# Performance work log

Hardware: AMD Instinct MI355X
Metric: run time of the kernel (lower is better)

The kernel has to match this reference:

```python
import jax, jax.numpy as jnp
import numpy as np
from jax.scipy.special import gammaln, digamma

V, H, K, B = 50000, 100, 50, 2048
BN_EPS = 1e-5
SAMPLE_KEY = jax.random.key(42)  # fixed key standing in for Dirichlet rsample noise


def setup_inputs() -> dict:
    key = jax.random.key(0)
    ks = jax.random.split(key, 6)
    def lin(k, fan_in, fan_out):
        bound = 1.0 / np.sqrt(fan_in)
        return jax.random.uniform(k, (fan_in, fan_out), jnp.float32, -bound, bound)
    return {
        'input_bows': jax.random.uniform(ks[0], (B, V), jnp.float32),  # BoW features
        'W1': lin(ks[1], V, H), 'b1': jnp.zeros((H,), jnp.float32),
        'W2': lin(ks[2], H, H), 'b2': jnp.zeros((H,), jnp.float32),
        'Wt': lin(ks[3], H, K), 'bt': jnp.zeros((K,), jnp.float32),
        'bn_gamma': jnp.ones((K,), jnp.float32), 'bn_beta': jnp.zeros((K,), jnp.float32),
        'Wd': lin(ks[4], K, V), 'bd': jnp.zeros((V,), jnp.float32),
    }


def reference(input_bows, W1, b1, W2, b2, Wt, bt, bn_gamma, bn_beta, Wd, bd):
    # --- MLP encoder: Linear -> Softplus, Linear -> Softplus ---
    h = jax.nn.softplus(input_bows @ W1 + b1)        # [B, H]
    h = jax.nn.softplus(h @ W2 + b2)                  # [B, H]
    # --- h2t: Linear -> BatchNorm1d (training-mode batch stats) -> exp ---
    t = h @ Wt + bt                                   # [B, K]
    mu = jnp.mean(t, axis=0)
    var = jnp.mean((t - mu) ** 2, axis=0)             # biased variance (torch BN)
    t_hat = (t - mu) * jax.lax.rsqrt(var + BN_EPS) * bn_gamma + bn_beta
    alpha = jnp.exp(t_hat)                            # Dirichlet concentration [B, K]
    # --- Dirichlet rsample: normalized Gamma (reparameterized) ---
    g = jax.random.gamma(SAMPLE_KEY, alpha)           # [B, K]
    sample = g / jnp.sum(g, axis=-1, keepdims=True)
    # --- decode: Linear -> log_softmax ---
    logits = jax.nn.log_softmax(sample @ Wd + bd, axis=-1)  # [B, V]
    rec_loss = -jnp.sum(logits * input_bows, axis=1)        # [B]
    # --- KL( Dirichlet(alpha) || Dirichlet(1) ) ---
    a0 = jnp.sum(alpha, axis=-1)                            # [B]
    kld = (gammaln(a0) - jnp.sum(gammaln(alpha), axis=-1) - gammaln(jnp.float32(K))
           + jnp.sum((alpha - 1.0) * (digamma(alpha) - digamma(a0)[:, None]), axis=-1))
    return sample, logits, kld, rec_loss
```

## Files before the change

### kernel.cpp

```cpp
#include <hip/hip_runtime.h>
#include <cstdint>
#include <cstddef>

#define DEV __device__ __forceinline__

struct TFKey { uint32_t a, b; };

DEV uint32_t rotl32(uint32_t x, uint32_t r){ return (x << r) | (x >> (32u - r)); }

DEV TFKey tf2x32(TFKey k, uint32_t x0, uint32_t x1){
  uint32_t ks0 = k.a, ks1 = k.b, ks2 = k.a ^ k.b ^ 0x1BD11BDAu;
  x0 += ks0; x1 += ks1;
  x0 += x1; x1 = rotl32(x1,13); x1 ^= x0;
  x0 += x1; x1 = rotl32(x1,15); x1 ^= x0;
  x0 += x1; x1 = rotl32(x1,26); x1 ^= x0;
  x0 += x1; x1 = rotl32(x1, 6); x1 ^= x0;
  x0 += ks1; x1 += ks2 + 1u;
  x0 += x1; x1 = rotl32(x1,17); x1 ^= x0;
  x0 += x1; x1 = rotl32(x1,29); x1 ^= x0;
  x0 += x1; x1 = rotl32(x1,16); x1 ^= x0;
  x0 += x1; x1 = rotl32(x1,24); x1 ^= x0;
  x0 += ks2; x1 += ks0 + 2u;
  x0 += x1; x1 = rotl32(x1,13); x1 ^= x0;
  x0 += x1; x1 = rotl32(x1,15); x1 ^= x0;
  x0 += x1; x1 = rotl32(x1,26); x1 ^= x0;
  x0 += x1; x1 = rotl32(x1, 6); x1 ^= x0;
  x0 += ks0; x1 += ks1 + 3u;
  x0 += x1; x1 = rotl32(x1,17); x1 ^= x0;
  x0 += x1; x1 = rotl32(x1,29); x1 ^= x0;
  x0 += x1; x1 = rotl32(x1,16); x1 ^= x0;
  x0 += x1; x1 = rotl32(x1,24); x1 ^= x0;
  x0 += ks1; x1 += ks2 + 4u;
  x0 += x1; x1 = rotl32(x1,13); x1 ^= x0;
  x0 += x1; x1 = rotl32(x1,15); x1 ^= x0;
  x0 += x1; x1 = rotl32(x1,26); x1 ^= x0;
  x0 += x1; x1 = rotl32(x1, 6); x1 ^= x0;
  x0 += ks2; x1 += ks0 + 5u;
  return TFKey{x0, x1};
}

DEV TFKey tf_child(TFKey k, uint32_t i){ return tf2x32(k, 0u, i); }
DEV uint32_t rb32(TFKey k){ TFKey o = tf2x32(k, 0u, 0u); return o.a ^ o.b; }

DEV float u01(TFKey k){
  uint32_t bits = rb32(k);
  return __uint_as_float((bits >> 9) | 0x3F800000u) - 1.0f;
}

DEV float cr_logf(float x){ return (float)log((double)x); }
DEV float cr_expf(float x){ return (float)exp((double)x); }
DEV float cr_powf(float x, float y){ return (float)pow((double)x, (double)y); }

DEV float xla_erfinv(float x){
  #pragma clang fp contract(off)
  float w = -(float)log1p((double)(-(x*x)));
  float p;
  if (w < 5.0f){
    w = w - 2.5f;
    p = 2.81022636e-08f;
    p = 3.43273939e-07f + p*w;
    p = -3.5233877e-06f + p*w;
    p = -4.39150654e-06f + p*w;
    p = 0.00021858087f  + p*w;
    p = -0.00125372503f + p*w;
    p = -0.00417768164f + p*w;
    p = 0.246640727f    + p*w;
    p = 1.50140941f     + p*w;
  } else {
    w = sqrtf(w) - 3.0f;
    p = -0.000200214257f;
    p = 0.000100950558f + p*w;
    p = 0.00134934322f  + p*w;
    p = -0.00367342844f + p*w;
    p = 0.00573950773f  + p*w;
    p = -0.0076224613f  + p*w;
    p = 0.00943887047f  + p*w;
    p = 1.00167406f     + p*w;
    p = 2.83297682f     + p*w;
  }
  return p*x;
}

DEV float normal_f(TFKey k){
  #pragma clang fp contract(off)
  uint32_t bits = rb32(k);
  float f = __uint_as_float((bits >> 9) | 0x3F800000u) - 1.0f;
  const float lo = -0x1.fffffep-1f;
  float u = f*2.0f + lo;
  u = fmaxf(lo, u);
  return 0x1.6a09e6p+0f * xla_erfinv(u);
}

DEV float gamma_one(TFKey ek, float alpha){
  #pragma clang fp contract(off)
  TFKey key = tf_child(ek, 0u);
  TFKey sub = tf_child(ek, 1u);
  bool bm = (alpha >= 1.0f);
  float a_orig = alpha;
  float ab = bm ? alpha : (alpha + 1.0f);
  const float c13 = 0x1.555556p-2f;
  float d = ab - c13;
  float c = c13 / sqrtf(d);
  float X = 0.0f, Vv = 1.0f, U = 2.0f;
  for (int it = 0; it < 1000; ++it){
    float sq = 1.0f - 0.0331f*(X*X);
    bool cont = false;
    if (U >= sq){
      float lV  = cr_logf(Vv);
      float rhs = 0.5f*X + ((d - d*Vv) + d*lV);
      cont = (cr_logf(U) >= rhs);
    }
    if (!cont) break;
    TFKey nk = tf_child(key, 0u);
    TFKey xk = tf_child(key, 1u);
    TFKey Uk = tf_child(key, 2u);
    key = nk;
    float x = 0.0f, v = -1.0f;
    for (int j = 0; j < 1000 && v <= 0.0f; ++j){
      TFKey nx = tf_child(xk, 0u);
      TFKey sk = tf_child(xk, 1u);
      xk = nx;
      x = normal_f(sk);
      v = 1.0f + x*c;
    }
    X = x*x;
    Vv = (v*v)*v;
    U = u01(Uk);
  }
  float boost = 1.0f;
  if (!bm) boost = cr_powf(u01(sub), 1.0f / a_orig);
  return (d*Vv)*boost;
}

DEV double digamma_d(double x){
  double r = 0.0;
  while (x < 6.0){ r -= 1.0/x; x += 1.0; }
  double ix = 1.0/x, ix2 = ix*ix;
  double ser = ix2*(1.0/12 - ix2*(1.0/120 - ix2*(1.0/252 - ix2*(1.0/240 - ix2*(1.0/132)))));
  return r + log(x) - 0.5*ix - ser;
}

DEV float softplus_cr(float x){
  double xd = (double)x;
  if (x > 0.0f) return (float)(xd + log1p(exp(-xd)));
  return (float)log1p(exp(xd));
}

__global__ __launch_bounds__(256) void k1_gemm(const float* __restrict__ bows,
                                               const float* __restrict__ W1,
                                               float* __restrict__ pre_part){
  __shared__ float4 At4[64*20];
  int rowb = blockIdx.x * 64;
  int kb   = blockIdx.y * 400;
  int tid  = threadIdx.x;
  int c    = tid & 31;
  int r8   = tid >> 5;
  float acc[8][4] = {};
  int cols[4];
  #pragma unroll
  for (int j = 0; j < 4; ++j){ int col = c + 32*j; cols[j] = col < 100 ? col : 96; }
  for (int t = 0; t < 5; ++t){
    int k0 = kb + t*80;
    #pragma unroll
    for (int j = 0; j < 5; ++j){
      int idx = tid + 256*j;
      int r = idx / 20, kf = idx - 20*r;
      At4[idx] = *(const float4*)(bows + (size_t)(rowb + r)*50000 + k0 + kf*4);
    }
    __syncthreads();
    const float* wbase = W1 + (size_t)k0 * 100;
    #pragma unroll 4
    for (int k4 = 0; k4 < 80; k4 += 4){
      float4 a[8];
      #pragma unroll
      for (int i = 0; i < 8; ++i) a[i] = At4[(r8 + 8*i)*20 + (k4 >> 2)];
      #pragma unroll
      for (int kk = 0; kk < 4; ++kk){
        const float* wr = wbase + (size_t)(k4 + kk)*100;
        float w[4];
        #pragma unroll
        for (int j = 0; j < 4; ++j) w[j] = wr[cols[j]];
        #pragma unroll
        for (int i = 0; i < 8; ++i){
          float av = (kk == 0) ? a[i].x : (kk == 1) ? a[i].y : (kk == 2) ? a[i].z : a[i].w;
          #pragma unroll
          for (int j = 0; j < 4; ++j) acc[i][j] = fmaf(av, w[j], acc[i][j]);
        }
      }
    }
    __syncthreads();
  }
  float* pp = pre_part + (size_t)blockIdx.y * 204800;
  #pragma unroll
  for (int i = 0; i < 8; ++i)
    #pragma unroll
    for (int j = 0; j < 4; ++j){
      int col = c + 32*j;
      if (col < 100) pp[(size_t)(rowb + r8 + 8*i)*100 + col] = acc[i][j];
    }
}

__global__ void k2a(const float* __restrict__ pre_part, const float* __restrict__ b1,
                    float* __restrict__ h1){
  int idx = blockIdx.x*256 + threadIdx.x;
  float s = 0.0f;
  #pragma unroll 5
  for (int sp = 0; sp < 125; ++sp) s += pre_part[(size_t)sp*204800 + idx];
  s += b1[idx % 100];
  h1[idx] = softplus_cr(s);
}

__global__ void k2b(const float* __restrict__ h1, const float* __restrict__ W2,
                    const float* __restrict__ b2, float* __restrict__ h2){
  int idx = blockIdx.x*256 + threadIdx.x;
  int row = idx / 100, c2 = idx - 100*row;
  float acc = 0.0f;
  for (int k = 0; k < 100; ++k) acc = fmaf(h1[row*100 + k], W2[k*100 + c2], acc);
  h2[idx] = softplus_cr(acc + b2[c2]);
}

__global__ void k2c(const float* __restrict__ h2, const float* __restrict__ Wt,
                    const float* __restrict__ bt, float* __restrict__ tbuf){
  int idx = blockIdx.x*256 + threadIdx.x;
  int row = idx / 50, c3 = idx - 50*row;
  float acc = 0.0f;
  for (int k = 0; k < 100; ++k) acc = fmaf(h2[row*100 + k], Wt[k*50 + c3], acc);
  tbuf[idx] = acc + bt[c3];
}

__global__ void k3_bn(const float* __restrict__ t, float* __restrict__ musig){
  int k = blockIdx.x, tid = threadIdx.x;
  __shared__ float red[256];
  float s = 0.0f;
  for (int r = tid; r < 2048; r += 256) s += t[r*50 + k];
  red[tid] = s; __syncthreads();
  for (int off = 128; off > 0; off >>= 1){ if (tid < off) red[tid] += red[tid+off]; __syncthreads(); }
  float mu = red[0] / 2048.0f;
  __syncthreads();
  float s2 = 0.0f;
  for (int r = tid; r < 2048; r += 256){ float d = t[r*50 + k] - mu; s2 += d*d; }
  red[tid] = s2; __syncthreads();
  for (int off = 128; off > 0; off >>= 1){ if (tid < off) red[tid] += red[tid+off]; __syncthreads(); }
  if (tid == 0){
    float var = red[0] / 2048.0f;
    musig[k] = mu;
    musig[64 + k] = (float)(1.0 / sqrt((double)(var + 1e-5f)));
  }
}

__global__ void k4_gamma(const float* __restrict__ t, const float* __restrict__ musig,
                         const float* __restrict__ bng, const float* __restrict__ bnb,
                         float* __restrict__ alpha_out, float* __restrict__ g_out){
  #pragma clang fp contract(off)
  int j = blockIdx.x*256 + threadIdx.x;
  int row = j / 50, k = j - 50*row; (void)row;
  float mu = musig[k], rs = musig[64 + k];
  float th = ((t[j] - mu) * rs) * bng[k] + bnb[k];
  float alpha = cr_expf(th);
  alpha_out[j] = alpha;
  TFKey master{0u, 42u};
  TFKey ek = tf2x32(master, 0u, (uint32_t)j);
  g_out[j] = gamma_one(ek, alpha);
}

__global__ void k5_row(const float* __restrict__ g, const float* __restrict__ alpha,
                       float* __restrict__ sample, float* __restrict__ kld){
  int lane = threadIdx.x & 63;
  int row = blockIdx.x*4 + (threadIdx.x >> 6);
  int base = row*50;
  float gv = (lane < 50) ? g[base + lane] : 0.0f;
  float av = (lane < 50) ? alpha[base + lane] : 0.0f;
  float sg = gv, a0 = av;
  for (int o = 32; o > 0; o >>= 1){ sg += __shfl_xor(sg, o, 64); a0 += __shfl_xor(a0, o, 64); }
  if (lane < 50) sample[base + lane] = gv / sg;
  double dga0 = digamma_d((double)a0);
  double gl = 0.0, tm = 0.0;
  if (lane < 50){
    double ad = (double)av;
    gl = lgamma(ad);
    tm = (ad - 1.0) * (digamma_d(ad) - dga0);
  }
  for (int o = 32; o > 0; o >>= 1){ gl += __shfl_xor(gl, o, 64); tm += __shfl_xor(tm, o, 64); }
  if (lane == 0)
    kld[row] = (float)(lgamma((double)a0) - gl - lgamma(50.0) + tm);
}


__global__ __launch_bounds__(256) void k6a(const float* __restrict__ sample,
                                           const float* __restrict__ Wd,
                                           const float* __restrict__ bd,
                                           const float* __restrict__ bows,
                                           double* __restrict__ part){
  __shared__ float s_lds[64*52];
  int rowb = blockIdx.x * 64;
  int colb = blockIdx.y * 256;
  int tid = threadIdx.x;
  for (int idx = tid; idx < 64*52; idx += 256){
    int r = idx / 52, k = idx - 52*r;
    s_lds[idx] = (k < 50) ? sample[(size_t)(rowb + r)*50 + k] : 0.0f;
  }
  __syncthreads();
  int lane = tid & 63, w = tid >> 6;
  int col = colb + 4*lane;
  bool act = col < 50000;
  float4 bd4 = {0.0f, 0.0f, 0.0f, 0.0f};
  if (act) bd4 = *(const float4*)(bd + col);
  for (int p = 0; p < 4; ++p){
    int r0 = w*16 + p*4;
    float4 acc[4] = {};
    const float* sb = s_lds + r0*52;
    if (act){
      #pragma unroll
      for (int q = 0; q < 12; ++q){
        #pragma unroll
        for (int kk = 0; kk < 4; ++kk){
          int k = q*4 + kk;
          float4 wd4 = *(const float4*)(Wd + (size_t)k*50000 + col);
          #pragma unroll
          for (int r = 0; r < 4; ++r){
            float sv = sb[r*52 + k];
            acc[r].x = fmaf(sv, wd4.x, acc[r].x);
            acc[r].y = fmaf(sv, wd4.y, acc[r].y);
            acc[r].z = fmaf(sv, wd4.z, acc[r].z);
            acc[r].w = fmaf(sv, wd4.w, acc[r].w);
          }
        }
      }
      #pragma unroll
      for (int kk = 0; kk < 2; ++kk){
        int k = 48 + kk;
        float4 wd4 = *(const float4*)(Wd + (size_t)k*50000 + col);
        #pragma unroll
        for (int r = 0; r < 4; ++r){
          float sv = sb[r*52 + k];
          acc[r].x = fmaf(sv, wd4.x, acc[r].x);
          acc[r].y = fmaf(sv, wd4.y, acc[r].y);
          acc[r].z = fmaf(sv, wd4.z, acc[r].z);
          acc[r].w = fmaf(sv, wd4.w, acc[r].w);
        }
      }
    }
    #pragma unroll
    for (int r = 0; r < 4; ++r){
      double se = 0.0, s1 = 0.0, sbw = 0.0;
      if (act){
        float4 bw = *(const float4*)(bows + (size_t)(rowb + r0 + r)*50000 + col);
        float zx = bd4.x + acc[r].x;
        float zy = bd4.y + acc[r].y;
        float zz = bd4.z + acc[r].z;
        float zw = bd4.w + acc[r].w;
        se  = ((double)expf(zx) + (double)expf(zy)) + ((double)expf(zz) + (double)expf(zw));
        s1  = (((double)zx*bw.x + (double)zy*bw.y) + ((double)zz*bw.z + (double)zw*bw.w));
        sbw = (((double)bw.x + (double)bw.y) + ((double)bw.z + (double)bw.w));
      }
      for (int o = 32; o > 0; o >>= 1){
        se  += __shfl_xor(se,  o, 64);
        s1  += __shfl_xor(s1,  o, 64);
        sbw += __shfl_xor(sbw, o, 64);
      }
      if (lane == 0){
        size_t off = ((size_t)(rowb + r0 + r)*196 + blockIdx.y)*3;
        part[off] = se; part[off+1] = s1; part[off+2] = sbw;
      }
    }
  }
}

__global__ void k6m(const double* __restrict__ part, float* __restrict__ lse,
                    float* __restrict__ rec){
  int row = blockIdx.x*256 + threadIdx.x;
  double se = 0, s1 = 0, sb = 0;
  const double* p = part + (size_t)row*588;
  for (int q = 0; q < 196; ++q){ se += p[3*q]; s1 += p[3*q+1]; sb += p[3*q+2]; }
  double l = log(se);
  lse[row] = (float)l;
  rec[row] = (float)(l*sb - s1);
}

__global__ __launch_bounds__(256) void k6b(const float* __restrict__ sample,
                                           const float* __restrict__ Wd,
                                           const float* __restrict__ bd,
                                           const float* __restrict__ lse,
                                           float* __restrict__ logits){
  __shared__ float s_lds[64*52];
  int rowb = blockIdx.x * 64;
  int colb = blockIdx.y * 256;
  int tid = threadIdx.x;
  for (int idx = tid; idx < 64*52; idx += 256){
    int r = idx / 52, k = idx - 52*r;
    s_lds[idx] = (k < 50) ? sample[(size_t)(rowb + r)*50 + k] : 0.0f;
  }
  __syncthreads();
  int lane = tid & 63, w = tid >> 6;
  int col = colb + 4*lane;
  bool act = col < 50000;
  float4 bd4 = {0.0f, 0.0f, 0.0f, 0.0f};
  if (act) bd4 = *(const float4*)(bd + col);
  for (int p = 0; p < 4; ++p){
    int r0 = w*16 + p*4;
    float4 acc[4] = {};
    const float* sb = s_lds + r0*52;
    if (act){
      #pragma unroll
      for (int q = 0; q < 12; ++q){
        #pragma unroll
        for (int kk = 0; kk < 4; ++kk){
          int k = q*4 + kk;
          float4 wd4 = *(const float4*)(Wd + (size_t)k*50000 + col);
          #pragma unroll
          for (int r = 0; r < 4; ++r){
            float sv = sb[r*52 + k];
            acc[r].x = fmaf(sv, wd4.x, acc[r].x);
            acc[r].y = fmaf(sv, wd4.y, acc[r].y);
            acc[r].z = fmaf(sv, wd4.z, acc[r].z);
            acc[r].w = fmaf(sv, wd4.w, acc[r].w);
          }
        }
      }
      #pragma unroll
      for (int kk = 0; kk < 2; ++kk){
        int k = 48 + kk;
        float4 wd4 = *(const float4*)(Wd + (size_t)k*50000 + col);
        #pragma unroll
        for (int r = 0; r < 4; ++r){
          float sv = sb[r*52 + k];
          acc[r].x = fmaf(sv, wd4.x, acc[r].x);
          acc[r].y = fmaf(sv, wd4.y, acc[r].y);
          acc[r].z = fmaf(sv, wd4.z, acc[r].z);
          acc[r].w = fmaf(sv, wd4.w, acc[r].w);
        }
      }
      #pragma unroll
      for (int r = 0; r < 4; ++r){
        float lf = lse[rowb + r0 + r];
        float4 z;
        z.x = (bd4.x + acc[r].x) - lf;
        z.y = (bd4.y + acc[r].y) - lf;
        z.z = (bd4.z + acc[r].z) - lf;
        z.w = (bd4.w + acc[r].w) - lf;
        *(float4*)(logits + (size_t)(rowb + r0 + r)*50000 + col) = z;
      }
    }
  }
}

extern "C" void kernel_launch(void* const* d_in, const int* in_sizes, int n_in,
                              void* d_out, int out_size, void* d_ws, size_t ws_size,
                              hipStream_t stream){
  (void)in_sizes; (void)n_in; (void)out_size; (void)ws_size;
  const float* bows = (const float*)d_in[0];
  const float* W1   = (const float*)d_in[1];
  const float* b1   = (const float*)d_in[2];
  const float* W2   = (const float*)d_in[3];
  const float* b2   = (const float*)d_in[4];
  const float* Wt   = (const float*)d_in[5];
  const float* bt   = (const float*)d_in[6];
  const float* bng  = (const float*)d_in[7];
  const float* bnb  = (const float*)d_in[8];
  const float* Wd   = (const float*)d_in[9];
  const float* bd   = (const float*)d_in[10];

  float* out    = (float*)d_out;
  float* sample = out;
  float* logits = out + 102400;
  float* kld    = out + 102400 + (size_t)2048*50000;
  float* rec    = kld + 2048;

  float*  pre_part = logits;
  float*  h1    = pre_part + (size_t)125*2048*100;
  float*  h2    = h1 + 204800;
  float*  tbuf  = h2 + 204800;
  float*  abuf  = tbuf + 102400;
  float*  gbuf  = abuf + 102400;
  float*  musig = gbuf + 102400;
  double* part  = (double*)(musig + 128);
  float*  lsew  = (float*)d_ws;

  k1_gemm<<<dim3(32, 125), 256, 0, stream>>>(bows, W1, pre_part);
  k2a<<<800, 256, 0, stream>>>(pre_part, b1, h1);
  k2b<<<800, 256, 0, stream>>>(h1, W2, b2, h2);
  k2c<<<400, 256, 0, stream>>>(h2, Wt, bt, tbuf);
  k3_bn<<<50, 256, 0, stream>>>(tbuf, musig);
  k4_gamma<<<400, 256, 0, stream>>>(tbuf, musig, bng, bnb, abuf, gbuf);
  k5_row<<<512, 256, 0, stream>>>(gbuf, abuf, sample, kld);
  k6a<<<dim3(32, 196), 256, 0, stream>>>(sample, Wd, bd, bows, part);
  k6m<<<8, 256, 0, stream>>>(part, lsew, rec);
  k6b<<<dim3(32, 196), 256, 0, stream>>>(sample, Wd, bd, lsew, logits);
}
```

Before: 1.068 ms.

## Write decoder logits once in k6a and subtract log-sum-exp in place

The decoder matmul is no longer recomputed in a second pass. k6a now writes the raw logits directly into the output while building the log-sum-exp and reconstruction partials. A new elementwise kernel then subtracts the per-row log-sum-exp in place. Each block now sweeps seven column tiles, which shrinks the partial array, so the partial buffers move into the workspace. This removes a full recompute of the small-K GEMM, but adds an extra read and write pass over the roughly 400 MB logits tensor and uses a smaller grid.

```diff
diff --git a/kernel.cpp b/kernel.cpp
--- a/kernel.cpp
+++ b/kernel.cpp
@@ -290,10 +290,11 @@
                                            const float* __restrict__ Wd,
                                            const float* __restrict__ bd,
                                            const float* __restrict__ bows,
+                                           float* __restrict__ zout,
                                            double* __restrict__ part){
   __shared__ float s_lds[64*52];
   int rowb = blockIdx.x * 64;
-  int colb = blockIdx.y * 256;
+  int tb0  = blockIdx.y * 7;
   int tid = threadIdx.x;
   for (int idx = tid; idx < 64*52; idx += 256){
     int r = idx / 52, k = idx - 52*r;
@@ -301,20 +302,17 @@
   }
   __syncthreads();
   int lane = tid & 63, w = tid >> 6;
-  int col = colb + 4*lane;
-  bool act = col < 50000;
-  float4 bd4 = {0.0f, 0.0f, 0.0f, 0.0f};
-  if (act) bd4 = *(const float4*)(bd + col);
   for (int p = 0; p < 4; ++p){
     int r0 = w*16 + p*4;
-    float4 acc[4] = {};
     const float* sb = s_lds + r0*52;
-    if (act){
-      #pragma unroll
-      for (int q = 0; q < 12; ++q){
-        #pragma unroll
-        for (int kk = 0; kk < 4; ++kk){
-          int k = q*4 + kk;
+    double se_l[4] = {}, s1_l[4] = {}, sb_l[4] = {};
+    for (int ct = 0; ct < 7; ++ct){
+      int col = (tb0 + ct)*256 + 4*lane;
+      if (col < 50000){
+        float4 bd4 = *(const float4*)(bd + col);
+        float4 acc[4] = {};
+        #pragma unroll 5
+        for (int k = 0; k < 50; ++k){
           float4 wd4 = *(const float4*)(Wd + (size_t)k*50000 + col);
           #pragma unroll
           for (int r = 0; r < 4; ++r){
@@ -325,41 +323,31 @@
             acc[r].w = fmaf(sv, wd4.w, acc[r].w);
           }
         }
-      }
-      #pragma unroll
-      for (int kk = 0; kk < 2; ++kk){
-        int k = 48 + kk;
-        float4 wd4 = *(const float4*)(Wd + (size_t)k*50000 + col);
         #pragma unroll
         for (int r = 0; r < 4; ++r){
-          float sv = sb[r*52 + k];
-          acc[r].x = fmaf(sv, wd4.x, acc[r].x);
-          acc[r].y = fmaf(sv, wd4.y, acc[r].y);
-          acc[r].z = fmaf(sv, wd4.z, acc[r].z);
-          acc[r].w = fmaf(sv, wd4.w, acc[r].w);
+          float4 bw = *(const float4*)(bows + (size_t)(rowb + r0 + r)*50000 + col);
+          float zx = bd4.x + acc[r].x;
+          float zy = bd4.y + acc[r].y;
+          float zz = bd4.z + acc[r].z;
+          float zw = bd4.w + acc[r].w;
+          float4 z4; z4.x = zx; z4.y = zy; z4.z = zz; z4.w = zw;
+          *(float4*)(zout + (size_t)(rowb + r0 + r)*50000 + col) = z4;
+          se_l[r] += ((double)expf(zx) + (double)expf(zy)) + ((double)expf(zz) + (double)expf(zw));
+          s1_l[r] += (((double)zx*bw.x + (double)zy*bw.y) + ((double)zz*bw.z + (double)zw*bw.w));
+          sb_l[r] += (((double)bw.x + (double)bw.y) + ((double)bw.z + (double)bw.w));
         }
       }
     }
     #pragma unroll
     for (int r = 0; r < 4; ++r){
-      double se = 0.0, s1 = 0.0, sbw = 0.0;
-      if (act){
-        float4 bw = *(const float4*)(bows + (size_t)(rowb + r0 + r)*50000 + col);
-        float zx = bd4.x + acc[r].x;
-        float zy = bd4.y + acc[r].y;
-        float zz = bd4.z + acc[r].z;
-        float zw = bd4.w + acc[r].w;
-        se  = ((double)expf(zx) + (double)expf(zy)) + ((double)expf(zz) + (double)expf(zw));
-        s1  = (((double)zx*bw.x + (double)zy*bw.y) + ((double)zz*bw.z + (double)zw*bw.w));
-        sbw = (((double)bw.x + (double)bw.y) + ((double)bw.z + (double)bw.w));
-      }
+      double se = se_l[r], s1 = s1_l[r], sbw = sb_l[r];
       for (int o = 32; o > 0; o >>= 1){
         se  += __shfl_xor(se,  o, 64);
         s1  += __shfl_xor(s1,  o, 64);
         sbw += __shfl_xor(sbw, o, 64);
       }
       if (lane == 0){
-        size_t off = ((size_t)(rowb + r0 + r)*196 + blockIdx.y)*3;
+        size_t off = ((size_t)(rowb + r0 + r)*28 + blockIdx.y)*3;
         part[off] = se; part[off+1] = s1; part[off+2] = sbw;
       }
     }
@@ -370,77 +358,24 @@
                     float* __restrict__ rec){
   int row = blockIdx.x*256 + threadIdx.x;
   double se = 0, s1 = 0, sb = 0;
-  const double* p = part + (size_t)row*588;
-  for (int q = 0; q < 196; ++q){ se += p[3*q]; s1 += p[3*q+1]; sb += p[3*q+2]; }
+  const double* p = part + (size_t)row*84;
+  for (int q = 0; q < 28; ++q){ se += p[3*q]; s1 += p[3*q+1]; sb += p[3*q+2]; }
   double l = log(se);
   lse[row] = (float)l;
   rec[row] = (float)(l*sb - s1);
 }
 
-__global__ __launch_bounds__(256) void k6b(const float* __restrict__ sample,
-                                           const float* __restrict__ Wd,
-                                           const float* __restrict__ bd,
-                                           const float* __restrict__ lse,
-                                           float* __restrict__ logits){
-  __shared__ float s_lds[64*52];
-  int rowb = blockIdx.x * 64;
-  int colb = blockIdx.y * 256;
-  int tid = threadIdx.x;
-  for (int idx = tid; idx < 64*52; idx += 256){
-    int r = idx / 52, k = idx - 52*r;
-    s_lds[idx] = (k < 50) ? sample[(size_t)(rowb + r)*50 + k] : 0.0f;
-  }
-  __syncthreads();
-  int lane = tid & 63, w = tid >> 6;
-  int col = colb + 4*lane;
-  bool act = col < 50000;
-  float4 bd4 = {0.0f, 0.0f, 0.0f, 0.0f};
-  if (act) bd4 = *(const float4*)(bd + col);
-  for (int p = 0; p < 4; ++p){
-    int r0 = w*16 + p*4;
-    float4 acc[4] = {};
-    const float* sb = s_lds + r0*52;
-    if (act){
-      #pragma unroll
-      for (int q = 0; q < 12; ++q){
-        #pragma unroll
-        for (int kk = 0; kk < 4; ++kk){
-          int k = q*4 + kk;
-          float4 wd4 = *(const float4*)(Wd + (size_t)k*50000 + col);
-          #pragma unroll
-          for (int r = 0; r < 4; ++r){
-            float sv = sb[r*52 + k];
-            acc[r].x = fmaf(sv, wd4.x, acc[r].x);
-            acc[r].y = fmaf(sv, wd4.y, acc[r].y);
-            acc[r].z = fmaf(sv, wd4.z, acc[r].z);
-            acc[r].w = fmaf(sv, wd4.w, acc[r].w);
-          }
-        }
-      }
-      #pragma unroll
-      for (int kk = 0; kk < 2; ++kk){
-        int k = 48 + kk;
-        float4 wd4 = *(const float4*)(Wd + (size_t)k*50000 + col);
-        #pragma unroll
-        for (int r = 0; r < 4; ++r){
-          float sv = sb[r*52 + k];
-          acc[r].x = fmaf(sv, wd4.x, acc[r].x);
-          acc[r].y = fmaf(sv, wd4.y, acc[r].y);
-          acc[r].z = fmaf(sv, wd4.z, acc[r].z);
-          acc[r].w = fmaf(sv, wd4.w, acc[r].w);
-        }
-      }
-      #pragma unroll
-      for (int r = 0; r < 4; ++r){
-        float lf = lse[rowb + r0 + r];
-        float4 z;
-        z.x = (bd4.x + acc[r].x) - lf;
-        z.y = (bd4.y + acc[r].y) - lf;
-        z.z = (bd4.z + acc[r].z) - lf;
-        z.w = (bd4.w + acc[r].w) - lf;
-        *(float4*)(logits + (size_t)(rowb + r0 + r)*50000 + col) = z;
-      }
-    }
+__global__ void k6z(float* __restrict__ logits, const float* __restrict__ lse){
+  size_t i = (size_t)blockIdx.x*256 + threadIdx.x;
+  const size_t n4 = 25600000;
+  size_t stride = (size_t)gridDim.x*256;
+  for (; i < n4; i += stride){
+    int row = (int)(i / 12500);
+    float lf = lse[row];
+    float4* p = (float4*)logits + i;
+    float4 z = *p;
+    z.x -= lf; z.y -= lf; z.z -= lf; z.w -= lf;
+    *p = z;
   }
 }
 
@@ -473,8 +408,8 @@
   float*  abuf  = tbuf + 102400;
   float*  gbuf  = abuf + 102400;
   float*  musig = gbuf + 102400;
-  double* part  = (double*)(musig + 128);
-  float*  lsew  = (float*)d_ws;
+  double* part  = (double*)d_ws;
+  float*  lsew  = (float*)(part + (size_t)2048*28*3);
 
   k1_gemm<<<dim3(32, 125), 256, 0, stream>>>(bows, W1, pre_part);
   k2a<<<800, 256, 0, stream>>>(pre_part, b1, h1);
@@ -483,7 +418,7 @@
   k3_bn<<<50, 256, 0, stream>>>(tbuf, musig);
   k4_gamma<<<400, 256, 0, stream>>>(tbuf, musig, bng, bnb, abuf, gbuf);
   k5_row<<<512, 256, 0, stream>>>(gbuf, abuf, sample, kld);
-  k6a<<<dim3(32, 196), 256, 0, stream>>>(sample, Wd, bd, bows, part);
+  k6a<<<dim3(32, 28), 256, 0, stream>>>(sample, Wd, bd, bows, logits, part);
   k6m<<<8, 256, 0, stream>>>(part, lsew, rec);
-  k6b<<<dim3(32, 196), 256, 0, stream>>>(sample, Wd, bd, lsew, logits);
-}
+  k6z<<<4096, 256, 0, stream>>>(logits, lsew);
+}
```

Result: slower. 1.262 ms (+18.1%).

## Store decoder logits in first pass and subtract log-sum-exp in place

Applied to the files above, without the earlier changes.

When the workspace is large enough, the first decode kernel now writes the raw logits z to the output buffer. A new elementwise kernel then subtracts the per-row log-sum-exp in place, replacing the second pass that recomputed the small K=50 decoder GEMM. Per-block partial sums are also stored as floats in the workspace instead of doubles. The trade adds a full extra read and write of the 2048x50000 logits matrix to save cheap recompute, and the float partials slightly reduce accumulation precision. The old two-pass path is kept as a fallback.

```diff
diff --git a/kernel.cpp b/kernel.cpp
--- a/kernel.cpp
+++ b/kernel.cpp
@@ -286,11 +286,12 @@
 }
 
 
-__global__ __launch_bounds__(256) void k6a(const float* __restrict__ sample,
-                                           const float* __restrict__ Wd,
-                                           const float* __restrict__ bd,
-                                           const float* __restrict__ bows,
-                                           double* __restrict__ part){
+__global__ __launch_bounds__(256) void k6a_f(const float* __restrict__ sample,
+                                             const float* __restrict__ Wd,
+                                             const float* __restrict__ bd,
+                                             const float* __restrict__ bows,
+                                             float* __restrict__ zout,
+                                             float* __restrict__ partF){
   __shared__ float s_lds[64*52];
   int rowb = blockIdx.x * 64;
   int colb = blockIdx.y * 256;
@@ -349,6 +350,8 @@
         float zy = bd4.y + acc[r].y;
         float zz = bd4.z + acc[r].z;
         float zw = bd4.w + acc[r].w;
+        float4 z4; z4.x = zx; z4.y = zy; z4.z = zz; z4.w = zw;
+        *(float4*)(zout + (size_t)(rowb + r0 + r)*50000 + col) = z4;
         se  = ((double)expf(zx) + (double)expf(zy)) + ((double)expf(zz) + (double)expf(zw));
         s1  = (((double)zx*bw.x + (double)zy*bw.y) + ((double)zz*bw.z + (double)zw*bw.w));
         sbw = (((double)bw.x + (double)bw.y) + ((double)bw.z + (double)bw.w));
@@ -360,28 +363,40 @@
       }
       if (lane == 0){
         size_t off = ((size_t)(rowb + r0 + r)*196 + blockIdx.y)*3;
-        part[off] = se; part[off+1] = s1; part[off+2] = sbw;
-      }
-    }
-  }
-}
-
-__global__ void k6m(const double* __restrict__ part, float* __restrict__ lse,
-                    float* __restrict__ rec){
+        partF[off] = (float)se; partF[off+1] = (float)s1; partF[off+2] = (float)sbw;
+      }
+    }
+  }
+}
+
+__global__ void k6m_f(const float* __restrict__ partF, float* __restrict__ lse,
+                      float* __restrict__ rec){
   int row = blockIdx.x*256 + threadIdx.x;
   double se = 0, s1 = 0, sb = 0;
-  const double* p = part + (size_t)row*588;
-  for (int q = 0; q < 196; ++q){ se += p[3*q]; s1 += p[3*q+1]; sb += p[3*q+2]; }
+  const float* p = partF + (size_t)row*588;
+  for (int q = 0; q < 196; ++q){ se += (double)p[3*q]; s1 += (double)p[3*q+1]; sb += (double)p[3*q+2]; }
   double l = log(se);
   lse[row] = (float)l;
   rec[row] = (float)(l*sb - s1);
 }
 
-__global__ __launch_bounds__(256) void k6b(const float* __restrict__ sample,
-                                           const float* __restrict__ Wd,
-                                           const float* __restrict__ bd,
-                                           const float* __restrict__ lse,
-                                           float* __restrict__ logits){
+__global__ void k6z(float* __restrict__ logits, const float* __restrict__ lse){
+  int row = blockIdx.y;
+  int col4 = blockIdx.x*256 + threadIdx.x;
+  if (col4 < 12500){
+    float lf = lse[row];
+    float4* p = (float4*)(logits + (size_t)row*50000) + col4;
+    float4 z = *p;
+    z.x -= lf; z.y -= lf; z.z -= lf; z.w -= lf;
+    *p = z;
+  }
+}
+
+__global__ __launch_bounds__(256) void k6a_sep(const float* __restrict__ sample,
+                                               const float* __restrict__ Wd,
+                                               const float* __restrict__ bd,
+                                               const float* __restrict__ bows,
+                                               double* __restrict__ part){
   __shared__ float s_lds[64*52];
   int rowb = blockIdx.x * 64;
   int colb = blockIdx.y * 256;
@@ -430,6 +445,97 @@
           acc[r].w = fmaf(sv, wd4.w, acc[r].w);
         }
       }
+    }
+    #pragma unroll
+    for (int r = 0; r < 4; ++r){
+      double se = 0.0, s1 = 0.0, sbw = 0.0;
+      if (act){
+        float4 bw = *(const float4*)(bows + (size_t)(rowb + r0 + r)*50000 + col);
+        float zx = bd4.x + acc[r].x;
+        float zy = bd4.y + acc[r].y;
+        float zz = bd4.z + acc[r].z;
+        float zw = bd4.w + acc[r].w;
+        se  = ((double)expf(zx) + (double)expf(zy)) + ((double)expf(zz) + (double)expf(zw));
+        s1  = (((double)zx*bw.x + (double)zy*bw.y) + ((double)zz*bw.z + (double)zw*bw.w));
+        sbw = (((double)bw.x + (double)bw.y) + ((double)bw.z + (double)bw.w));
+      }
+      for (int o = 32; o > 0; o >>= 1){
+        se  += __shfl_xor(se,  o, 64);
+        s1  += __shfl_xor(s1,  o, 64);
+        sbw += __shfl_xor(sbw, o, 64);
+      }
+      if (lane == 0){
+        size_t off = ((size_t)(rowb + r0 + r)*196 + blockIdx.y)*3;
+        part[off] = se; part[off+1] = s1; part[off+2] = sbw;
+      }
+    }
+  }
+}
+
+__global__ void k6m_d(const double* __restrict__ part, float* __restrict__ lse,
+                      float* __restrict__ rec){
+  int row = blockIdx.x*256 + threadIdx.x;
+  double se = 0, s1 = 0, sb = 0;
+  const double* p = part + (size_t)row*588;
+  for (int q = 0; q < 196; ++q){ se += p[3*q]; s1 += p[3*q+1]; sb += p[3*q+2]; }
+  double l = log(se);
+  lse[row] = (float)l;
+  rec[row] = (float)(l*sb - s1);
+}
+
+__global__ __launch_bounds__(256) void k6b_sep(const float* __restrict__ sample,
+                                               const float* __restrict__ Wd,
+                                               const float* __restrict__ bd,
+                                               const float* __restrict__ lse,
+                                               float* __restrict__ logits){
+  __shared__ float s_lds[64*52];
+  int rowb = blockIdx.x * 64;
+  int colb = blockIdx.y * 256;
+  int tid = threadIdx.x;
+  for (int idx = tid; idx < 64*52; idx += 256){
+    int r = idx / 52, k = idx - 52*r;
+    s_lds[idx] = (k < 50) ? sample[(size_t)(rowb + r)*50 + k] : 0.0f;
+  }
+  __syncthreads();
+  int lane = tid & 63, w = tid >> 6;
+  int col = colb + 4*lane;
+  bool act = col < 50000;
+  float4 bd4 = {0.0f, 0.0f, 0.0f, 0.0f};
+  if (act) bd4 = *(const float4*)(bd + col);
+  for (int p = 0; p < 4; ++p){
+    int r0 = w*16 + p*4;
+    float4 acc[4] = {};
+    const float* sb = s_lds + r0*52;
+    if (act){
+      #pragma unroll
+      for (int q = 0; q < 12; ++q){
+        #pragma unroll
+        for (int kk = 0; kk < 4; ++kk){
+          int k = q*4 + kk;
+          float4 wd4 = *(const float4*)(Wd + (size_t)k*50000 + col);
+          #pragma unroll
+          for (int r = 0; r < 4; ++r){
+            float sv = sb[r*52 + k];
+            acc[r].x = fmaf(sv, wd4.x, acc[r].x);
+            acc[r].y = fmaf(sv, wd4.y, acc[r].y);
+            acc[r].z = fmaf(sv, wd4.z, acc[r].z);
+            acc[r].w = fmaf(sv, wd4.w, acc[r].w);
+          }
+        }
+      }
+      #pragma unroll
+      for (int kk = 0; kk < 2; ++kk){
+        int k = 48 + kk;
+        float4 wd4 = *(const float4*)(Wd + (size_t)k*50000 + col);
+        #pragma unroll
+        for (int r = 0; r < 4; ++r){
+          float sv = sb[r*52 + k];
+          acc[r].x = fmaf(sv, wd4.x, acc[r].x);
+          acc[r].y = fmaf(sv, wd4.y, acc[r].y);
+          acc[r].z = fmaf(sv, wd4.z, acc[r].z);
+          acc[r].w = fmaf(sv, wd4.w, acc[r].w);
+        }
+      }
       #pragma unroll
       for (int r = 0; r < 4; ++r){
         float lf = lse[rowb + r0 + r];
@@ -447,7 +553,7 @@
 extern "C" void kernel_launch(void* const* d_in, const int* in_sizes, int n_in,
                               void* d_out, int out_size, void* d_ws, size_t ws_size,
                               hipStream_t stream){
-  (void)in_sizes; (void)n_in; (void)out_size; (void)ws_size;
+  (void)in_sizes; (void)n_in; (void)out_size;
   const float* bows = (const float*)d_in[0];
   const float* W1   = (const float*)d_in[1];
   const float* b1   = (const float*)d_in[2];
@@ -473,8 +579,6 @@
   float*  abuf  = tbuf + 102400;
   float*  gbuf  = abuf + 102400;
   float*  musig = gbuf + 102400;
-  double* part  = (double*)(musig + 128);
-  float*  lsew  = (float*)d_ws;
 
   k1_gemm<<<dim3(32, 125), 256, 0, stream>>>(bows, W1, pre_part);
   k2a<<<800, 256, 0, stream>>>(pre_part, b1, h1);
@@ -483,7 +587,19 @@
   k3_bn<<<50, 256, 0, stream>>>(tbuf, musig);
   k4_gamma<<<400, 256, 0, stream>>>(tbuf, musig, bng, bnb, abuf, gbuf);
   k5_row<<<512, 256, 0, stream>>>(gbuf, abuf, sample, kld);
-  k6a<<<dim3(32, 196), 256, 0, stream>>>(sample, Wd, bd, bows, part);
-  k6m<<<8, 256, 0, stream>>>(part, lsew, rec);
-  k6b<<<dim3(32, 196), 256, 0, stream>>>(sample, Wd, bd, lsew, logits);
-}
+
+  const size_t needF = (size_t)2048*196*3*sizeof(float) + 2048*sizeof(float);
+  if (ws_size >= needF){
+    float* partF = (float*)d_ws;
+    float* lsew  = partF + (size_t)2048*196*3;
+    k6a_f<<<dim3(32, 196), 256, 0, stream>>>(sample, Wd, bd, bows, logits, partF);
+    k6m_f<<<8, 256, 0, stream>>>(partF, lsew, rec);
+    k6z<<<dim3(49, 2048), 256, 0, stream>>>(logits, lsew);
+  } else {
+    double* partD = (double*)(musig + 128);
+    float*  lsew  = (float*)d_ws;
+    k6a_sep<<<dim3(32, 196), 256, 0, stream>>>(sample, Wd, bd, bows, partD);
+    k6m_d<<<8, 256, 0, stream>>>(partD, lsew, rec);
+    k6b_sep<<<dim3(32, 196), 256, 0, stream>>>(sample, Wd, bd, lsew, logits);
+  }
+}
```

After: 1.040 ms. 1.03x faster.
